# Kernel optimization log

Measured on AMD Instinct MI355X. Metric: run time of the kernel, lower is better.

Reference implementation:

```python
import jax, jax.numpy as jnp
import numpy as np

N_NODES = 100000
N_EDGES = 1600000
N_GRAPHS = 1000
H = 128
F_IN = 128
F_EDGE = 16
DEPTH = 4


def setup_inputs() -> dict:
    key = jax.random.key(0)
    ks = jax.random.split(key, 10)
    s = 1.0 / np.sqrt(H)
    x = jax.random.normal(ks[0], (N_NODES, F_IN), dtype=jnp.float32)
    edge_index = jax.random.randint(ks[1], (2, N_EDGES), 0, N_NODES, dtype=jnp.int32)
    edge_attr = jax.random.normal(ks[2], (N_EDGES, F_EDGE), dtype=jnp.float32)
    batch = jnp.sort(jax.random.randint(ks[3], (N_NODES,), 0, N_GRAPHS, dtype=jnp.int32))
    W0 = jax.random.normal(ks[4], (F_IN, H), dtype=jnp.float32) * s
    b0 = jnp.zeros((H,), dtype=jnp.float32)
    W1 = jax.random.normal(ks[5], (DEPTH, H, H), dtype=jnp.float32) * s
    b1 = jnp.zeros((DEPTH, H), dtype=jnp.float32)
    W2 = jax.random.normal(ks[6], (DEPTH, H, H), dtype=jnp.float32) * s
    b2 = jnp.zeros((DEPTH, H), dtype=jnp.float32)
    Wf = jax.random.normal(ks[7], (H, 1), dtype=jnp.float32) * s
    bf = jnp.zeros((1,), dtype=jnp.float32)
    return {"x": x, "edge_index": edge_index, "edge_attr": edge_attr, "batch": batch,
            "W0": W0, "b0": b0, "W1": W1, "b1": b1, "W2": W2, "b2": b2, "Wf": Wf, "bf": bf}


def reference(x, edge_index, edge_attr, batch, W0, b0, W1, b1, W2, b2, Wf, bf):
    # edge_attr is read by the original forward but never used in the math.
    src, dst = edge_index[0], edge_index[1]
    n = x.shape[0]
    h0 = jax.nn.relu(x @ W0 + b0)  # [N, H]
    h = h0
    for i in range(DEPTH):
        # GINConv (eps=0): MLP(x + sum_{j in N(i)} x_j); messages flow src -> dst
        agg = jax.ops.segment_sum(h[src], dst, num_segments=n)  # [N, H]
        z = h + agg
        z = jax.nn.relu(z @ W1[i] + b1[i]) @ W2[i] + b2[i]
        # residual then relu (dropout p=0.02 is identity at eval)
        h = jax.nn.relu(z + h0)
    pooled = jax.ops.segment_sum(h, batch, num_segments=N_GRAPHS)  # [G, H]
    out = (pooled @ Wf + bf)[:, 0]  # [G]
    return out
```

## Files before the change

kernel.cpp:

```cpp
#include <hip/hip_runtime.h>

#define N_NODES 100000
#define N_EDGES 1600000
#define N_GRAPHS 1000
#define H 128
#define DEPTH 4
#define NB 391
#define BCAP 4864
#define WPITCH 136
#define WSLOT (H * WPITCH)

typedef __attribute__((ext_vector_type(8))) short bf16x8;
typedef __attribute__((ext_vector_type(4))) float f32x4;

__device__ __forceinline__ unsigned short f2bf(float f) {
  unsigned int u = __float_as_uint(f);
  u += 0x7FFF + ((u >> 16) & 1);
  return (unsigned short)(u >> 16);
}
__device__ __forceinline__ float bflo(unsigned int v) { return __uint_as_float(v << 16); }
__device__ __forceinline__ float bfhi(unsigned int v) { return __uint_as_float(v & 0xFFFF0000u); }

__global__ __launch_bounds__(256) void k_bcnt(const int* __restrict__ dst, int* __restrict__ gcnt) {
  __shared__ int c[NB];
  int tid = threadIdx.x, e0 = blockIdx.x * 4096;
  for (int i = tid; i < NB; i += 256) c[i] = 0;
  __syncthreads();
#pragma unroll
  for (int i = 0; i < 16; ++i) {
    int e = e0 + i * 256 + tid;
    if (e < N_EDGES) atomicAdd(&c[dst[e] >> 8], 1);
  }
  __syncthreads();
  for (int i = tid; i < NB; i += 256)
    if (c[i]) atomicAdd(&gcnt[i], c[i]);
}

__global__ __launch_bounds__(512) void k_bscan(const int* __restrict__ gcnt, int* __restrict__ boff,
                                               int* __restrict__ cursor) {
  __shared__ int sh[512];
  int t = threadIdx.x;
  int v = (t < NB) ? gcnt[t] : 0;
  sh[t] = v;
  __syncthreads();
  for (int s = 1; s < 512; s <<= 1) {
    int x = (t >= s) ? sh[t - s] : 0;
    __syncthreads();
    sh[t] += x;
    __syncthreads();
  }
  if (t < NB) {
    int e = sh[t] - v;
    boff[t] = e;
    cursor[t] = e;
  }
  if (t == 0) boff[NB] = N_EDGES;
}

__global__ __launch_bounds__(256) void k_bucket(const int* __restrict__ src, const int* __restrict__ dst,
                                                int* __restrict__ cursor, unsigned int* __restrict__ ebuf) {
  __shared__ int cnt[NB];
  __shared__ int base[NB];
  int tid = threadIdx.x;
  int e0 = blockIdx.x * 4096;
  for (int i = tid; i < NB; i += 256) cnt[i] = 0;
  __syncthreads();
  unsigned int pk[16];
  int bk[16], rk[16];
#pragma unroll
  for (int i = 0; i < 16; ++i) {
    int e = e0 + i * 256 + tid;
    if (e < N_EDGES) {
      int s = src[e], d = dst[e];
      bk[i] = d >> 8;
      pk[i] = ((unsigned int)(d & 255) << 17) | (unsigned int)s;
      rk[i] = atomicAdd(&cnt[bk[i]], 1);
    } else
      bk[i] = -1;
  }
  __syncthreads();
  for (int i = tid; i < NB; i += 256)
    base[i] = cnt[i] ? atomicAdd(&cursor[i], cnt[i]) : 0;
  __syncthreads();
#pragma unroll
  for (int i = 0; i < 16; ++i)
    if (bk[i] >= 0) ebuf[base[bk[i]] + rk[i]] = pk[i];
}

__global__ __launch_bounds__(256) void k_bsort(const unsigned int* __restrict__ ebuf,
                                               const int* __restrict__ boff,
                                               int* __restrict__ csr, int* __restrict__ offs) {
  __shared__ unsigned int arr[BCAP];
  __shared__ unsigned int srt[BCAP];
  __shared__ unsigned short rnk[BCAP];
  __shared__ int cnt[256];
  __shared__ int off[257];
  int b = blockIdx.x, tid = threadIdx.x;
  int beg = boff[b], end = boff[b + 1];
  int ce = min(end - beg, BCAP);
  cnt[tid] = 0;
  __syncthreads();
  for (int i = tid; i < ce; i += 256) {
    unsigned int p = ebuf[beg + i];
    arr[i] = p;
    rnk[i] = (unsigned short)atomicAdd(&cnt[p >> 17], 1);
  }
  __syncthreads();
  int v = cnt[tid];
  off[tid + 1] = v;
  if (tid == 0) off[0] = 0;
  __syncthreads();
  for (int s = 1; s < 256; s <<= 1) {
    int x = (tid + 1 > s) ? off[tid + 1 - s] : 0;
    __syncthreads();
    off[tid + 1] += x;
    __syncthreads();
  }
  for (int i = tid; i < ce; i += 256) {
    unsigned int p = arr[i];
    srt[off[p >> 17] + rnk[i]] = p & 0x1FFFF;
  }
  __syncthreads();
  for (int i = tid; i < ce; i += 256) csr[beg + i] = (int)srt[i];
  int node = (b << 8) + tid;
  if (node < N_NODES) offs[node] = beg + off[tid];
  if (b == NB - 1 && tid == 0) offs[N_NODES] = N_EDGES;
}

__global__ __launch_bounds__(256) void k_wprep(const float* __restrict__ W0, const float* __restrict__ W1,
                                               const float* __restrict__ W2, unsigned short* __restrict__ wb) {
  int m = blockIdx.x >> 3, part = blockIdx.x & 7, tid = threadIdx.x;
  const float* src = (m == 0) ? W0 : ((m <= DEPTH) ? W1 + (size_t)(m - 1) * H * H : W2 + (size_t)(m - 1 - DEPTH) * H * H);
  unsigned short* dst = wb + (size_t)m * WSLOT;
  int idx = part * 256 + tid;
  int ng4 = idx & 31, kp = idx >> 5;
  float4 r0 = *(const float4*)&src[(2 * kp) * H + 4 * ng4];
  float4 r1 = *(const float4*)&src[(2 * kp + 1) * H + 4 * ng4];
  unsigned int p0 = (unsigned int)f2bf(r0.x) | ((unsigned int)f2bf(r1.x) << 16);
  unsigned int p1 = (unsigned int)f2bf(r0.y) | ((unsigned int)f2bf(r1.y) << 16);
  unsigned int p2 = (unsigned int)f2bf(r0.z) | ((unsigned int)f2bf(r1.z) << 16);
  unsigned int p3 = (unsigned int)f2bf(r0.w) | ((unsigned int)f2bf(r1.w) << 16);
  *(unsigned int*)&dst[(4 * ng4 + 0) * WPITCH + 2 * kp] = p0;
  *(unsigned int*)&dst[(4 * ng4 + 1) * WPITCH + 2 * kp] = p1;
  *(unsigned int*)&dst[(4 * ng4 + 2) * WPITCH + 2 * kp] = p2;
  *(unsigned int*)&dst[(4 * ng4 + 3) * WPITCH + 2 * kp] = p3;
}

__device__ __forceinline__ void stage_wb(const unsigned short* __restrict__ Wg, unsigned short* Wt, int tid) {
#pragma unroll
  for (int i = 0; i < 4; ++i) {
    int c = tid + i * 512;
    *(uint4*)&Wt[c * 8] = *(const uint4*)&Wg[c * 8];
  }
  int c = tid + 2048;
  if (c < 2176) *(uint4*)&Wt[c * 8] = *(const uint4*)&Wg[c * 8];
}

__global__ __launch_bounds__(512) void k_lin(const float* __restrict__ in, const unsigned short* __restrict__ w0t,
                                             const float* __restrict__ bg, unsigned short* __restrict__ outp) {
  __shared__ __align__(16) unsigned short Wt[WSLOT];
  __shared__ __align__(16) unsigned short zs[128 * 136];
  int tid = threadIdx.x;
  int lane = tid & 63, w = tid >> 6;
  int q = lane >> 4, l16 = lane & 15;
  int n0 = blockIdx.x * 128;

  stage_wb(w0t, Wt, tid);

  int row = n0 + w * 16 + l16;
  int rr = (row < N_NODES) ? row : 0;
  bf16x8 afrag[4];
#pragma unroll
  for (int ks = 0; ks < 4; ++ks) {
    const float* p = &in[(size_t)rr * H + ks * 32 + q * 8];
    float4 f0 = *(const float4*)p;
    float4 f1 = *(const float4*)(p + 4);
    bf16x8 a;
    a[0] = (short)f2bf(f0.x); a[1] = (short)f2bf(f0.y); a[2] = (short)f2bf(f0.z); a[3] = (short)f2bf(f0.w);
    a[4] = (short)f2bf(f1.x); a[5] = (short)f2bf(f1.y); a[6] = (short)f2bf(f1.z); a[7] = (short)f2bf(f1.w);
    afrag[ks] = a;
  }
  f32x4 acc[8];
#pragma unroll
  for (int ct = 0; ct < 8; ++ct) acc[ct] = (f32x4){0.f, 0.f, 0.f, 0.f};
  __syncthreads();
#pragma unroll
  for (int ct = 0; ct < 8; ++ct)
#pragma unroll
    for (int ks = 0; ks < 4; ++ks) {
      bf16x8 b = *(bf16x8*)&Wt[(ct * 16 + l16) * WPITCH + ks * 32 + q * 8];
      acc[ct] = __builtin_amdgcn_mfma_f32_16x16x32_bf16(afrag[ks], b, acc[ct], 0, 0, 0);
    }
#pragma unroll
  for (int ct = 0; ct < 8; ++ct) {
    float bb = bg[ct * 16 + l16];
#pragma unroll
    for (int r = 0; r < 4; ++r) {
      float v = fmaxf(acc[ct][r] + bb, 0.f);
      zs[(w * 16 + q * 4 + r) * 136 + ct * 16 + l16] = f2bf(v);
    }
  }
  __syncthreads();
  int node = tid >> 2, cb = (tid & 3) * 32;
  if (n0 + node < N_NODES) {
#pragma unroll
    for (int i = 0; i < 4; ++i) {
      uint4 v = *(uint4*)&zs[node * 136 + cb + i * 8];
      *(uint4*)&outp[(size_t)(n0 + node) * H + cb + i * 8] = v;
    }
  }
}

__global__ __launch_bounds__(256) void k_agg(const unsigned short* __restrict__ hin, const int* __restrict__ offs,
                                             const int* __restrict__ csr, unsigned short* __restrict__ zin) {
  int node = blockIdx.x * 8 + (threadIdx.x >> 5);
  int l = threadIdx.x & 31;
  if (node >= N_NODES) return;
  const uint2* hu = (const uint2*)hin;
  uint2 self = hu[(size_t)node * 32 + l];
  float a0 = bflo(self.x), a1 = bfhi(self.x), a2 = bflo(self.y), a3 = bfhi(self.y);
  int beg = offs[node], end = offs[node + 1];
  for (int e = beg; e < end; e += 32) {
    int cnt = min(32, end - e);
    int idx = (l < cnt) ? csr[e + l] : 0;
    int j = 0;
    for (; j + 8 <= cnt; j += 8) {
      int s0 = __shfl(idx, j, 32), s1 = __shfl(idx, j + 1, 32);
      int s2 = __shfl(idx, j + 2, 32), s3 = __shfl(idx, j + 3, 32);
      int s4 = __shfl(idx, j + 4, 32), s5 = __shfl(idx, j + 5, 32);
      int s6 = __shfl(idx, j + 6, 32), s7 = __shfl(idx, j + 7, 32);
      uint2 v0 = hu[(size_t)s0 * 32 + l];
      uint2 v1 = hu[(size_t)s1 * 32 + l];
      uint2 v2 = hu[(size_t)s2 * 32 + l];
      uint2 v3 = hu[(size_t)s3 * 32 + l];
      uint2 v4 = hu[(size_t)s4 * 32 + l];
      uint2 v5 = hu[(size_t)s5 * 32 + l];
      uint2 v6 = hu[(size_t)s6 * 32 + l];
      uint2 v7 = hu[(size_t)s7 * 32 + l];
      a0 += bflo(v0.x); a1 += bfhi(v0.x); a2 += bflo(v0.y); a3 += bfhi(v0.y);
      a0 += bflo(v1.x); a1 += bfhi(v1.x); a2 += bflo(v1.y); a3 += bfhi(v1.y);
      a0 += bflo(v2.x); a1 += bfhi(v2.x); a2 += bflo(v2.y); a3 += bfhi(v2.y);
      a0 += bflo(v3.x); a1 += bfhi(v3.x); a2 += bflo(v3.y); a3 += bfhi(v3.y);
      a0 += bflo(v4.x); a1 += bfhi(v4.x); a2 += bflo(v4.y); a3 += bfhi(v4.y);
      a0 += bflo(v5.x); a1 += bfhi(v5.x); a2 += bflo(v5.y); a3 += bfhi(v5.y);
      a0 += bflo(v6.x); a1 += bfhi(v6.x); a2 += bflo(v6.y); a3 += bfhi(v6.y);
      a0 += bflo(v7.x); a1 += bfhi(v7.x); a2 += bflo(v7.y); a3 += bfhi(v7.y);
    }
    for (; j + 4 <= cnt; j += 4) {
      int s0 = __shfl(idx, j, 32), s1 = __shfl(idx, j + 1, 32);
      int s2 = __shfl(idx, j + 2, 32), s3 = __shfl(idx, j + 3, 32);
      uint2 v0 = hu[(size_t)s0 * 32 + l];
      uint2 v1 = hu[(size_t)s1 * 32 + l];
      uint2 v2 = hu[(size_t)s2 * 32 + l];
      uint2 v3 = hu[(size_t)s3 * 32 + l];
      a0 += bflo(v0.x); a1 += bfhi(v0.x); a2 += bflo(v0.y); a3 += bfhi(v0.y);
      a0 += bflo(v1.x); a1 += bfhi(v1.x); a2 += bflo(v1.y); a3 += bfhi(v1.y);
      a0 += bflo(v2.x); a1 += bfhi(v2.x); a2 += bflo(v2.y); a3 += bfhi(v2.y);
      a0 += bflo(v3.x); a1 += bfhi(v3.x); a2 += bflo(v3.y); a3 += bfhi(v3.y);
    }
    for (; j < cnt; ++j) {
      int s = __shfl(idx, j, 32);
      uint2 v = hu[(size_t)s * 32 + l];
      a0 += bflo(v.x); a1 += bfhi(v.x); a2 += bflo(v.y); a3 += bfhi(v.y);
    }
  }
  unsigned long long o = (unsigned long long)((unsigned int)f2bf(a0) | ((unsigned int)f2bf(a1) << 16)) |
                         ((unsigned long long)((unsigned int)f2bf(a2) | ((unsigned int)f2bf(a3) << 16)) << 32);
  __builtin_nontemporal_store(o, (unsigned long long*)zin + (size_t)node * 32 + l);
}

__global__ __launch_bounds__(512) void k_mlp(const unsigned short* __restrict__ zin,
                                             const unsigned short* __restrict__ w1t, const float* __restrict__ b1g,
                                             const unsigned short* __restrict__ w2t, const float* __restrict__ b2g,
                                             const unsigned short* __restrict__ h0, unsigned short* __restrict__ h) {
  __shared__ __align__(16) unsigned short Wt[WSLOT];
  __shared__ __align__(16) unsigned short zs[128 * 136];
  int tid = threadIdx.x;
  int lane = tid & 63, w = tid >> 6;
  int q = lane >> 4, l16 = lane & 15;
  int n0 = blockIdx.x * 128;

  stage_wb(w1t, Wt, tid);

  int row = n0 + w * 16 + l16;
  int rr = (row < N_NODES) ? row : 0;
  bf16x8 afrag[4];
#pragma unroll
  for (int ks = 0; ks < 4; ++ks)
    afrag[ks] = *(bf16x8*)&zin[(size_t)rr * H + ks * 32 + q * 8];

  f32x4 acc[8];
#pragma unroll
  for (int ct = 0; ct < 8; ++ct) acc[ct] = (f32x4){0.f, 0.f, 0.f, 0.f};
  __syncthreads();
#pragma unroll
  for (int ct = 0; ct < 8; ++ct)
#pragma unroll
    for (int ks = 0; ks < 4; ++ks) {
      bf16x8 b = *(bf16x8*)&Wt[(ct * 16 + l16) * WPITCH + ks * 32 + q * 8];
      acc[ct] = __builtin_amdgcn_mfma_f32_16x16x32_bf16(afrag[ks], b, acc[ct], 0, 0, 0);
    }
  __syncthreads();
  stage_wb(w2t, Wt, tid);
#pragma unroll
  for (int ct = 0; ct < 8; ++ct) {
    float bb = b1g[ct * 16 + l16];
#pragma unroll
    for (int r = 0; r < 4; ++r) {
      float v = fmaxf(acc[ct][r] + bb, 0.f);
      zs[(w * 16 + q * 4 + r) * 136 + ct * 16 + l16] = f2bf(v);
    }
  }
  __syncthreads();
  bf16x8 a2[4];
#pragma unroll
  for (int ks = 0; ks < 4; ++ks)
    a2[ks] = *(bf16x8*)&zs[(w * 16 + l16) * 136 + ks * 32 + q * 8];
  f32x4 acc2[8];
#pragma unroll
  for (int ct = 0; ct < 8; ++ct) acc2[ct] = (f32x4){0.f, 0.f, 0.f, 0.f};
#pragma unroll
  for (int ct = 0; ct < 8; ++ct)
#pragma unroll
    for (int ks = 0; ks < 4; ++ks) {
      bf16x8 b = *(bf16x8*)&Wt[(ct * 16 + l16) * WPITCH + ks * 32 + q * 8];
      acc2[ct] = __builtin_amdgcn_mfma_f32_16x16x32_bf16(a2[ks], b, acc2[ct], 0, 0, 0);
    }
#pragma unroll
  for (int ct = 0; ct < 8; ++ct) {
    float bb = b2g[ct * 16 + l16];
#pragma unroll
    for (int r = 0; r < 4; ++r) {
      float v = acc2[ct][r] + bb;
      zs[(w * 16 + q * 4 + r) * 136 + ct * 16 + l16] = f2bf(v);
    }
  }
  __syncthreads();
  int node = tid >> 2, cb = (tid & 3) * 32;
  if (n0 + node < N_NODES) {
    size_t base = (size_t)(n0 + node) * H + cb;
#pragma unroll
    for (int i = 0; i < 4; ++i) {
      uint4 zv = *(uint4*)&zs[node * 136 + cb + i * 8];
      uint4 hv = *(const uint4*)&h0[base + i * 8];
      unsigned int zr[4] = {zv.x, zv.y, zv.z, zv.w};
      unsigned int hr[4] = {hv.x, hv.y, hv.z, hv.w};
      uint4 o;
      unsigned int orr[4];
#pragma unroll
      for (int j = 0; j < 4; ++j) {
        float a = fmaxf(bflo(zr[j]) + bflo(hr[j]), 0.f);
        float b = fmaxf(bfhi(zr[j]) + bfhi(hr[j]), 0.f);
        orr[j] = (unsigned int)f2bf(a) | ((unsigned int)f2bf(b) << 16);
      }
      o.x = orr[0]; o.y = orr[1]; o.z = orr[2]; o.w = orr[3];
      *(uint4*)&h[base + i * 8] = o;
    }
  }
}

__global__ void k_starts(const int* __restrict__ batch, int* __restrict__ starts) {
  int n = blockIdx.x * 256 + threadIdx.x;
  if (n >= N_NODES) return;
  int b = batch[n];
  if (n == 0) {
    for (int g = 0; g <= b; ++g) starts[g] = 0;
  } else {
    int bp = batch[n - 1];
    for (int g = bp + 1; g <= b; ++g) starts[g] = n;
  }
  if (n == N_NODES - 1) {
    for (int g = b + 1; g <= N_GRAPHS; ++g) starts[g] = N_NODES;
  }
}

__global__ __launch_bounds__(256) void k_pool(const unsigned short* __restrict__ h, const int* __restrict__ starts,
                                              const float* __restrict__ Wf, const float* __restrict__ bf_,
                                              float* __restrict__ out) {
  __shared__ float r[4];
  int g = blockIdx.x, tid = threadIdx.x;
  int lane = tid & 63, w = tid >> 6;
  int beg = starts[g], end = starts[g + 1];
  const unsigned int* hu = (const unsigned int*)h;
  float sx = 0.f, sy = 0.f;
  for (int n = beg + w; n < end; n += 4) {
    unsigned int v = hu[(size_t)n * 64 + lane];
    sx += bflo(v);
    sy += bfhi(v);
  }
  float val = sx * Wf[2 * lane] + sy * Wf[2 * lane + 1];
#pragma unroll
  for (int off = 32; off > 0; off >>= 1) val += __shfl_down(val, off);
  if (lane == 0) r[w] = val;
  __syncthreads();
  if (tid == 0) out[g] = r[0] + r[1] + r[2] + r[3] + bf_[0];
}

extern "C" void kernel_launch(void* const* d_in, const int* in_sizes, int n_in,
                              void* d_out, int out_size, void* d_ws, size_t ws_size,
                              hipStream_t stream) {
  const float* x = (const float*)d_in[0];
  const int* ei = (const int*)d_in[1];
  const int* srcv = ei;
  const int* dstv = ei + N_EDGES;
  const int* batch = (const int*)d_in[3];
  const float* W0 = (const float*)d_in[4];
  const float* b0 = (const float*)d_in[5];
  const float* W1 = (const float*)d_in[6];
  const float* b1 = (const float*)d_in[7];
  const float* W2 = (const float*)d_in[8];
  const float* b2 = (const float*)d_in[9];
  const float* Wf = (const float*)d_in[10];
  const float* bf_ = (const float*)d_in[11];
  float* out = (float*)d_out;

  char* ws = (char*)d_ws;
  size_t o = 0;
  auto alloc = [&](size_t bytes) {
    size_t r = o;
    o = (o + bytes + 255) & ~(size_t)255;
    return r;
  };
  int* offs = (int*)(ws + alloc((N_NODES + 1) * sizeof(int)));
  int* gcnt = (int*)(ws + alloc(NB * sizeof(int)));
  int* boff = (int*)(ws + alloc((NB + 1) * sizeof(int)));
  int* cursor = (int*)(ws + alloc(NB * sizeof(int)));
  unsigned int* ebuf = (unsigned int*)(ws + alloc((size_t)N_EDGES * 4));
  int* csr = (int*)(ws + alloc((size_t)N_EDGES * sizeof(int)));
  int* starts = (int*)(ws + alloc((N_GRAPHS + 1) * sizeof(int)));
  unsigned short* h0 = (unsigned short*)(ws + alloc((size_t)N_NODES * H * 2));
  unsigned short* h = (unsigned short*)(ws + alloc((size_t)N_NODES * H * 2));
  unsigned short* zin = (unsigned short*)(ws + alloc((size_t)N_NODES * H * 2));
  unsigned short* wbuf = (unsigned short*)(ws + alloc((size_t)9 * WSLOT * 2));

  hipMemsetAsync(gcnt, 0, NB * sizeof(int), stream);
  k_wprep<<<72, 256, 0, stream>>>(W0, W1, W2, wbuf);
  k_bcnt<<<NB, 256, 0, stream>>>(dstv, gcnt);
  k_bscan<<<1, 512, 0, stream>>>(gcnt, boff, cursor);
  k_bucket<<<NB, 256, 0, stream>>>(srcv, dstv, cursor, ebuf);
  k_bsort<<<NB, 256, 0, stream>>>(ebuf, boff, csr, offs);
  k_starts<<<(N_NODES + 255) / 256, 256, 0, stream>>>(batch, starts);

  const int nblk = (N_NODES + 127) / 128;
  k_lin<<<nblk, 512, 0, stream>>>(x, wbuf, b0, h0);
  for (int i = 0; i < DEPTH; ++i) {
    const unsigned short* hin = (i == 0) ? h0 : h;
    k_agg<<<(N_NODES + 7) / 8, 256, 0, stream>>>(hin, offs, csr, zin);
    k_mlp<<<nblk, 512, 0, stream>>>(zin, wbuf + (size_t)(1 + i) * WSLOT, b1 + (size_t)i * H,
                                    wbuf + (size_t)(1 + DEPTH + i) * WSLOT, b2 + (size_t)i * H,
                                    h0, h);
  }
  k_pool<<<N_GRAPHS, 256, 0, stream>>>(h, starts, Wf, bf_, out);
}
```

Measured before the change: 601.4 us.

## Fuse neighbor aggregation into MLP kernel with ping-pong hidden buffers

```diff
diff --git a/kernel.cpp b/kernel.cpp
--- a/kernel.cpp
+++ b/kernel.cpp
@@ -211,88 +211,91 @@
   }
 }
 
-__global__ __launch_bounds__(256) void k_agg(const unsigned short* __restrict__ hin, const int* __restrict__ offs,
-                                             const int* __restrict__ csr, unsigned short* __restrict__ zin) {
-  int node = blockIdx.x * 8 + (threadIdx.x >> 5);
-  int l = threadIdx.x & 31;
-  if (node >= N_NODES) return;
-  const uint2* hu = (const uint2*)hin;
-  uint2 self = hu[(size_t)node * 32 + l];
-  float a0 = bflo(self.x), a1 = bfhi(self.x), a2 = bflo(self.y), a3 = bfhi(self.y);
-  int beg = offs[node], end = offs[node + 1];
-  for (int e = beg; e < end; e += 32) {
-    int cnt = min(32, end - e);
-    int idx = (l < cnt) ? csr[e + l] : 0;
-    int j = 0;
-    for (; j + 8 <= cnt; j += 8) {
-      int s0 = __shfl(idx, j, 32), s1 = __shfl(idx, j + 1, 32);
-      int s2 = __shfl(idx, j + 2, 32), s3 = __shfl(idx, j + 3, 32);
-      int s4 = __shfl(idx, j + 4, 32), s5 = __shfl(idx, j + 5, 32);
-      int s6 = __shfl(idx, j + 6, 32), s7 = __shfl(idx, j + 7, 32);
-      uint2 v0 = hu[(size_t)s0 * 32 + l];
-      uint2 v1 = hu[(size_t)s1 * 32 + l];
-      uint2 v2 = hu[(size_t)s2 * 32 + l];
-      uint2 v3 = hu[(size_t)s3 * 32 + l];
-      uint2 v4 = hu[(size_t)s4 * 32 + l];
-      uint2 v5 = hu[(size_t)s5 * 32 + l];
-      uint2 v6 = hu[(size_t)s6 * 32 + l];
-      uint2 v7 = hu[(size_t)s7 * 32 + l];
-      a0 += bflo(v0.x); a1 += bfhi(v0.x); a2 += bflo(v0.y); a3 += bfhi(v0.y);
-      a0 += bflo(v1.x); a1 += bfhi(v1.x); a2 += bflo(v1.y); a3 += bfhi(v1.y);
-      a0 += bflo(v2.x); a1 += bfhi(v2.x); a2 += bflo(v2.y); a3 += bfhi(v2.y);
-      a0 += bflo(v3.x); a1 += bfhi(v3.x); a2 += bflo(v3.y); a3 += bfhi(v3.y);
-      a0 += bflo(v4.x); a1 += bfhi(v4.x); a2 += bflo(v4.y); a3 += bfhi(v4.y);
-      a0 += bflo(v5.x); a1 += bfhi(v5.x); a2 += bflo(v5.y); a3 += bfhi(v5.y);
-      a0 += bflo(v6.x); a1 += bfhi(v6.x); a2 += bflo(v6.y); a3 += bfhi(v6.y);
-      a0 += bflo(v7.x); a1 += bfhi(v7.x); a2 += bflo(v7.y); a3 += bfhi(v7.y);
-    }
-    for (; j + 4 <= cnt; j += 4) {
-      int s0 = __shfl(idx, j, 32), s1 = __shfl(idx, j + 1, 32);
-      int s2 = __shfl(idx, j + 2, 32), s3 = __shfl(idx, j + 3, 32);
-      uint2 v0 = hu[(size_t)s0 * 32 + l];
-      uint2 v1 = hu[(size_t)s1 * 32 + l];
-      uint2 v2 = hu[(size_t)s2 * 32 + l];
-      uint2 v3 = hu[(size_t)s3 * 32 + l];
-      a0 += bflo(v0.x); a1 += bfhi(v0.x); a2 += bflo(v0.y); a3 += bfhi(v0.y);
-      a0 += bflo(v1.x); a1 += bfhi(v1.x); a2 += bflo(v1.y); a3 += bfhi(v1.y);
-      a0 += bflo(v2.x); a1 += bfhi(v2.x); a2 += bflo(v2.y); a3 += bfhi(v2.y);
-      a0 += bflo(v3.x); a1 += bfhi(v3.x); a2 += bflo(v3.y); a3 += bfhi(v3.y);
-    }
-    for (; j < cnt; ++j) {
-      int s = __shfl(idx, j, 32);
-      uint2 v = hu[(size_t)s * 32 + l];
-      a0 += bflo(v.x); a1 += bfhi(v.x); a2 += bflo(v.y); a3 += bfhi(v.y);
-    }
-  }
-  unsigned long long o = (unsigned long long)((unsigned int)f2bf(a0) | ((unsigned int)f2bf(a1) << 16)) |
-                         ((unsigned long long)((unsigned int)f2bf(a2) | ((unsigned int)f2bf(a3) << 16)) << 32);
-  __builtin_nontemporal_store(o, (unsigned long long*)zin + (size_t)node * 32 + l);
-}
-
-__global__ __launch_bounds__(512) void k_mlp(const unsigned short* __restrict__ zin,
+#define ACC8(v)                                                       \
+  {                                                                   \
+    a0 += bflo(v.x); a1 += bfhi(v.x); a2 += bflo(v.y); a3 += bfhi(v.y); \
+    a4 += bflo(v.z); a5 += bfhi(v.z); a6 += bflo(v.w); a7 += bfhi(v.w); \
+  }
+
+__global__ __launch_bounds__(512) void k_mlp(const unsigned short* __restrict__ hin,
+                                             const int* __restrict__ offs, const int* __restrict__ csr,
                                              const unsigned short* __restrict__ w1t, const float* __restrict__ b1g,
                                              const unsigned short* __restrict__ w2t, const float* __restrict__ b2g,
-                                             const unsigned short* __restrict__ h0, unsigned short* __restrict__ h) {
+                                             const unsigned short* __restrict__ h0, unsigned short* __restrict__ hout) {
   __shared__ __align__(16) unsigned short Wt[WSLOT];
   __shared__ __align__(16) unsigned short zs[128 * 136];
   int tid = threadIdx.x;
+  int n0 = blockIdx.x * 128;
+
+  stage_wb(w1t, Wt, tid);
+
+  {
+    int g = tid >> 4, l = tid & 15;
+    const uint4* hu4 = (const uint4*)hin;
+    for (int it = 0; it < 4; ++it) {
+      int nl = g * 4 + it;
+      int node = n0 + nl;
+      int nc = (node < N_NODES) ? node : 0;
+      uint4 self = hu4[(size_t)nc * 16 + l];
+      float a0 = bflo(self.x), a1 = bfhi(self.x), a2 = bflo(self.y), a3 = bfhi(self.y);
+      float a4 = bflo(self.z), a5 = bfhi(self.z), a6 = bflo(self.w), a7 = bfhi(self.w);
+      int beg = offs[nc], end = offs[nc + 1];
+      if (node >= N_NODES) end = beg;
+      for (int e = beg; e < end; e += 16) {
+        int cnt = min(16, end - e);
+        int idx = (l < cnt) ? csr[e + l] : 0;
+        int j = 0;
+        for (; j + 8 <= cnt; j += 8) {
+          int s0 = __shfl(idx, j, 16), s1 = __shfl(idx, j + 1, 16);
+          int s2 = __shfl(idx, j + 2, 16), s3 = __shfl(idx, j + 3, 16);
+          int s4 = __shfl(idx, j + 4, 16), s5 = __shfl(idx, j + 5, 16);
+          int s6 = __shfl(idx, j + 6, 16), s7 = __shfl(idx, j + 7, 16);
+          uint4 v0 = hu4[(size_t)s0 * 16 + l];
+          uint4 v1 = hu4[(size_t)s1 * 16 + l];
+          uint4 v2 = hu4[(size_t)s2 * 16 + l];
+          uint4 v3 = hu4[(size_t)s3 * 16 + l];
+          uint4 v4 = hu4[(size_t)s4 * 16 + l];
+          uint4 v5 = hu4[(size_t)s5 * 16 + l];
+          uint4 v6 = hu4[(size_t)s6 * 16 + l];
+          uint4 v7 = hu4[(size_t)s7 * 16 + l];
+          ACC8(v0) ACC8(v1) ACC8(v2) ACC8(v3) ACC8(v4) ACC8(v5) ACC8(v6) ACC8(v7)
+        }
+        for (; j + 4 <= cnt; j += 4) {
+          int s0 = __shfl(idx, j, 16), s1 = __shfl(idx, j + 1, 16);
+          int s2 = __shfl(idx, j + 2, 16), s3 = __shfl(idx, j + 3, 16);
+          uint4 v0 = hu4[(size_t)s0 * 16 + l];
+          uint4 v1 = hu4[(size_t)s1 * 16 + l];
+          uint4 v2 = hu4[(size_t)s2 * 16 + l];
+          uint4 v3 = hu4[(size_t)s3 * 16 + l];
+          ACC8(v0) ACC8(v1) ACC8(v2) ACC8(v3)
+        }
+        for (; j < cnt; ++j) {
+          int s = __shfl(idx, j, 16);
+          uint4 v = hu4[(size_t)s * 16 + l];
+          ACC8(v)
+        }
+      }
+      unsigned int o0 = (unsigned int)f2bf(a0) | ((unsigned int)f2bf(a1) << 16);
+      unsigned int o1 = (unsigned int)f2bf(a2) | ((unsigned int)f2bf(a3) << 16);
+      unsigned int o2 = (unsigned int)f2bf(a4) | ((unsigned int)f2bf(a5) << 16);
+      unsigned int o3 = (unsigned int)f2bf(a6) | ((unsigned int)f2bf(a7) << 16);
+      uint4 o;
+      o.x = o0; o.y = o1; o.z = o2; o.w = o3;
+      *(uint4*)&zs[nl * 136 + l * 8] = o;
+    }
+  }
+  __syncthreads();
+
   int lane = tid & 63, w = tid >> 6;
   int q = lane >> 4, l16 = lane & 15;
-  int n0 = blockIdx.x * 128;
-
-  stage_wb(w1t, Wt, tid);
-
-  int row = n0 + w * 16 + l16;
-  int rr = (row < N_NODES) ? row : 0;
   bf16x8 afrag[4];
 #pragma unroll
   for (int ks = 0; ks < 4; ++ks)
-    afrag[ks] = *(bf16x8*)&zin[(size_t)rr * H + ks * 32 + q * 8];
+    afrag[ks] = *(bf16x8*)&zs[(w * 16 + l16) * 136 + ks * 32 + q * 8];
 
   f32x4 acc[8];
 #pragma unroll
   for (int ct = 0; ct < 8; ++ct) acc[ct] = (f32x4){0.f, 0.f, 0.f, 0.f};
-  __syncthreads();
 #pragma unroll
   for (int ct = 0; ct < 8; ++ct)
 #pragma unroll
@@ -312,6 +315,7 @@
     }
   }
   __syncthreads();
+
   bf16x8 a2[4];
 #pragma unroll
   for (int ks = 0; ks < 4; ++ks)
@@ -354,7 +358,7 @@
         orr[j] = (unsigned int)f2bf(a) | ((unsigned int)f2bf(b) << 16);
       }
       o.x = orr[0]; o.y = orr[1]; o.z = orr[2]; o.w = orr[3];
-      *(uint4*)&h[base + i * 8] = o;
+      *(uint4*)&hout[base + i * 8] = o;
     }
   }
 }
@@ -429,8 +433,8 @@
   int* csr = (int*)(ws + alloc((size_t)N_EDGES * sizeof(int)));
   int* starts = (int*)(ws + alloc((N_GRAPHS + 1) * sizeof(int)));
   unsigned short* h0 = (unsigned short*)(ws + alloc((size_t)N_NODES * H * 2));
-  unsigned short* h = (unsigned short*)(ws + alloc((size_t)N_NODES * H * 2));
-  unsigned short* zin = (unsigned short*)(ws + alloc((size_t)N_NODES * H * 2));
+  unsigned short* hA = (unsigned short*)(ws + alloc((size_t)N_NODES * H * 2));
+  unsigned short* hB = (unsigned short*)(ws + alloc((size_t)N_NODES * H * 2));
   unsigned short* wbuf = (unsigned short*)(ws + alloc((size_t)9 * WSLOT * 2));
 
   hipMemsetAsync(gcnt, 0, NB * sizeof(int), stream);
@@ -444,11 +448,12 @@
   const int nblk = (N_NODES + 127) / 128;
   k_lin<<<nblk, 512, 0, stream>>>(x, wbuf, b0, h0);
   for (int i = 0; i < DEPTH; ++i) {
-    const unsigned short* hin = (i == 0) ? h0 : h;
-    k_agg<<<(N_NODES + 7) / 8, 256, 0, stream>>>(hin, offs, csr, zin);
-    k_mlp<<<nblk, 512, 0, stream>>>(zin, wbuf + (size_t)(1 + i) * WSLOT, b1 + (size_t)i * H,
+    const unsigned short* hin = (i == 0) ? h0 : ((i & 1) ? hA : hB);
+    unsigned short* hout = (i & 1) ? hB : hA;
+    k_mlp<<<nblk, 512, 0, stream>>>(hin, offs, csr,
+                                    wbuf + (size_t)(1 + i) * WSLOT, b1 + (size_t)i * H,
                                     wbuf + (size_t)(1 + DEPTH + i) * WSLOT, b2 + (size_t)i * H,
-                                    h0, h);
-  }
-  k_pool<<<N_GRAPHS, 256, 0, stream>>>(h, starts, Wf, bf_, out);
-}
+                                    h0, hout);
+  }
+  k_pool<<<N_GRAPHS, 256, 0, stream>>>(hB, starts, Wf, bf_, out);
+}
```

Result: no change. 596.9 us (-0.7%).
